# Performance work log

Hardware: AMD Instinct MI355X
Metric: run time of the kernel (lower is better)

The kernel has to match this reference:

```python
import jax, jax.numpy as jnp
import numpy as np
from math import sqrt

P = 1.0  # axis-aligned transform exponent (init arg p)
EPS = 1e-6


def setup_inputs() -> dict:
    key = jax.random.key(0)
    k1, k2, k3, k4 = jax.random.split(key, 4)
    B, L, S, H, E = 4, 2048, 2048, 8, 64
    return {
        "queries": jax.random.normal(k1, (B, L, H, E), dtype=jnp.float32),
        "keys": jax.random.normal(k2, (B, S, H, E), dtype=jnp.float32),
        "values": jax.random.normal(k3, (B, S, H, E), dtype=jnp.float32),
        "attn_mask": jnp.zeros((1, 1, 1, 1), dtype=bool),  # unused: mask_flag=False
        "directional_weights": jnp.ones((1, 1, 1, 1), dtype=jnp.float32),
        "dynamic_param": jax.random.normal(k4, (1,), dtype=jnp.float32),
    }


def _transform(x, directional_weights, dynamic_param):
    # axis_aligned_transformation: rescale by (1/std over seq dim)^p (unbiased std, like torch)
    std = jnp.std(x, axis=-2, keepdims=True, ddof=1)
    x = x * (1.0 / (std + EPS)) ** P
    # directional_reweighting then nonlinear_mapping
    x = x * directional_weights
    return jnp.tanh(x) * dynamic_param


def reference(queries, keys, values, attn_mask, directional_weights, dynamic_param):
    B, L, H, E = queries.shape
    scale = 1.0 / sqrt(E)
    qt = _transform(queries, directional_weights, dynamic_param)  # [B,L,H,E]
    kt = _transform(keys, directional_weights, dynamic_param)     # [B,S,H,E]
    scores = jnp.einsum('blhe,bshe->bhls', qt, kt)                # [B,H,L,S]
    # per-row tau = sqrt(var(scores) + eps), unbiased variance like torch.var
    tau = jnp.sqrt(jnp.var(scores, axis=-1, keepdims=True, ddof=1) + EPS)
    A = jax.nn.softmax(scale * scores / tau, axis=-1)             # [B,H,L,S]
    V = jnp.einsum('bhls,bshd->blhd', A, values)                  # [B,L,H,D]
    return V
```

## Files before the change

### kernel.cpp

```cpp
#include <hip/hip_runtime.h>
#include <math.h>

#define B_ 4
#define L_ 2048
#define S_ 2048
#define H_ 8
#define E_ 64
#define BH_ (B_*H_)
#define EPS 1e-6f

typedef __attribute__((ext_vector_type(8))) short short8;
typedef __attribute__((ext_vector_type(4))) float f32x4;

__device__ __forceinline__ unsigned short f2bf(float f) {
    unsigned int u = __float_as_uint(f);
    u = (u + 0x7fffu + ((u >> 16) & 1u)) >> 16;
    return (unsigned short)u;
}

__device__ __forceinline__ float bf2f(unsigned short u) {
    return __uint_as_float(((unsigned int)u) << 16);
}

__device__ __forceinline__ float fast_tanh(float x) {
    float e = __expf(2.0f * x);
    return 1.0f - 2.0f / (e + 1.0f);
}

__device__ __forceinline__ int swb(int row, int byteoff) {
    return row * 128 + ((((byteoff >> 4) ^ (row & 7)) << 4) | (byteoff & 15));
}

__global__ __launch_bounds__(256) void pre_kernel(
    const float* __restrict__ xq, const float* __restrict__ xk,
    const float* __restrict__ xv,
    unsigned short* __restrict__ qt, unsigned short* __restrict__ kt,
    unsigned short* __restrict__ vt,
    const float* __restrict__ dwp, const float* __restrict__ dpp)
{
    __shared__ float ls[64][65];
    int bx = blockIdx.x;
    if (bx < 4096) {
        const float* x = (bx < 2048) ? xq : xk;
        unsigned short* xt = (bx < 2048) ? qt : kt;
        int g = (bx & 2047) * 256 + threadIdx.x;
        int e = g & 63;
        int bl = g >> 6;
        int b = bl >> 11;
        int l = bl & 2047;
        size_t base = (size_t)bl * (H_ * E_) + e;
        float v[8], s = 0.f, q = 0.f;
#pragma unroll
        for (int h = 0; h < 8; ++h) {
            float t = x[base + h * E_];
            v[h] = t; s += t; q += t * t;
        }
        float mean = s * 0.125f;
        float var = (q - s * mean) * (1.f / 7.f);
        var = fmaxf(var, 0.f);
        float inv = 1.f / (sqrtf(var) + EPS);
        float wsc = dwp[0] * inv;
        float d = dpp[0];
#pragma unroll
        for (int h = 0; h < 8; ++h) {
            float t = fast_tanh(v[h] * wsc) * d;
            xt[((size_t)(b * H_ + h) * L_ + l) * E_ + e] = f2bf(t);
        }
    } else {
        int t2 = bx - 4096;
        int s0 = (t2 & 31) * 64;
        int h = (t2 >> 5) & 7, b = t2 >> 8;
        int t = threadIdx.x;
#pragma unroll
        for (int i = 0; i < 4; ++i) {
            int idx = t + i * 256;
            int r = idx >> 4, c4 = (idx & 15) * 4;
            const float4 f = *(const float4*)&xv[((size_t)(b * S_ + s0 + r) * H_ + h) * E_ + c4];
            ls[r][c4] = f.x; ls[r][c4 + 1] = f.y; ls[r][c4 + 2] = f.z; ls[r][c4 + 3] = f.w;
        }
        __syncthreads();
        size_t ob = ((size_t)(b * H_ + h) * (S_ / 64) + (s0 >> 6)) * 4096;
#pragma unroll
        for (int i = 0; i < 2; ++i) {
            int ri = t + i * 256;
            int et = ri >> 7, c = (ri >> 6) & 1, quad = (ri >> 4) & 3, m = ri & 15;
            int e = et * 16 + m, sb = c * 32 + quad * 8;
            unsigned short tmp[8];
#pragma unroll
            for (int j = 0; j < 8; ++j) tmp[j] = f2bf(ls[sb + j][e]);
            *(uint4*)&vt[ob + (size_t)ri * 8] = *(uint4*)tmp;
        }
    }
}

__global__ __launch_bounds__(256) void gram_kernel(
    const unsigned short* __restrict__ kt, unsigned short* __restrict__ Gb,
    float* __restrict__ ksum)
{
    __shared__ unsigned short ks[128 * 72];
    __shared__ float gs[4096];
    __shared__ float kss[64];
    int bh = blockIdx.x;
    const unsigned short* base = kt + (size_t)bh * S_ * E_;
    int tid = threadIdx.x, lane = tid & 63, w = tid >> 6;
    int m = lane & 15, quad = lane >> 4;

    f32x4 acc[4][4];
#pragma unroll
    for (int i = 0; i < 4; ++i)
#pragma unroll
        for (int j = 0; j < 4; ++j) acc[i][j] = (f32x4){0.f, 0.f, 0.f, 0.f};
    float ksp[4] = {0.f, 0.f, 0.f, 0.f};

    short8 stg[4];
#pragma unroll
    for (int i = 0; i < 4; ++i)
        stg[i] = *(const short8*)(base + (size_t)(tid + i * 256) * 8);

    for (int ch = 0; ch < 16; ++ch) {
        __syncthreads();
#pragma unroll
        for (int i = 0; i < 4; ++i) {
            int u = tid + i * 256;
            *(short8*)&ks[(u >> 3) * 72 + (u & 7) * 8] = stg[i];
        }
        __syncthreads();
        if (ch < 15) {
#pragma unroll
            for (int i = 0; i < 4; ++i)
                stg[i] = *(const short8*)(base + (size_t)(ch + 1) * 8192 + (tid + i * 256) * 8);
        }
        int s0 = w * 32;
        short8 af[4];
#pragma unroll
        for (int i = 0; i < 4; ++i) {
            short8 a;
#pragma unroll
            for (int kk = 0; kk < 8; ++kk) {
                unsigned short uv = ks[(s0 + quad * 8 + kk) * 72 + i * 16 + m];
                a[kk] = (short)uv;
                ksp[i] += bf2f(uv);
            }
            af[i] = a;
        }
#pragma unroll
        for (int i = 0; i < 4; ++i)
#pragma unroll
            for (int j = 0; j < 4; ++j)
                acc[i][j] = __builtin_amdgcn_mfma_f32_16x16x32_bf16(af[i], af[j], acc[i][j], 0, 0, 0);
    }
#pragma unroll
    for (int i = 0; i < 4; ++i) {
        ksp[i] += __shfl_xor(ksp[i], 16);
        ksp[i] += __shfl_xor(ksp[i], 32);
    }
    for (int w2 = 0; w2 < 4; ++w2) {
        if (w == w2) {
#pragma unroll
            for (int i = 0; i < 4; ++i)
#pragma unroll
                for (int j = 0; j < 4; ++j)
#pragma unroll
                    for (int r = 0; r < 4; ++r) {
                        int idx = (i * 16 + quad * 4 + r) * 64 + j * 16 + m;
                        if (w2 == 0) gs[idx] = acc[i][j][r]; else gs[idx] += acc[i][j][r];
                    }
            if (lane < 16) {
#pragma unroll
                for (int i = 0; i < 4; ++i) {
                    int e = i * 16 + lane;
                    if (w2 == 0) kss[e] = ksp[i]; else kss[e] += ksp[i];
                }
            }
        }
        __syncthreads();
    }
#pragma unroll
    for (int ii = 0; ii < 16; ++ii) {
        int idx = tid + ii * 256;
        Gb[(size_t)bh * 4096 + idx] = f2bf(gs[idx]);
    }
    if (tid < 64) ksum[bh * 64 + tid] = kss[tid];
}

__global__ __launch_bounds__(512, 4) void attn_kernel(
    const unsigned short* __restrict__ qt,
    const unsigned short* __restrict__ kt,
    const unsigned short* __restrict__ vt,
    const unsigned short* __restrict__ Gb,
    const float* __restrict__ ksum,
    float* __restrict__ out)
{
    __shared__ __align__(16) char lds[33792];
    const int tid = threadIdx.x;
    const int lane = tid & 63;
    const int w = tid >> 6;
    const int m = lane & 15;
    const int quad = lane >> 4;
    char* ptb = lds + 16384 + w * 2048;
    float2* ascr = (float2*)(lds + 32768) + w * 16;

    int blk = blockIdx.x;
    int bh = (blk & 7) * 4 + ((blk >> 3) & 3);
    int l0 = (blk >> 5) * 128;
    int b = bh >> 3, h = bh & 7;

    const unsigned short* qtb = qt + (size_t)bh * L_ * E_;
    const unsigned short* ktb = kt + (size_t)bh * S_ * E_;
    const unsigned short* vtb = vt + (size_t)bh * (S_ / 64) * 4096;

    short8 qf[2];
#pragma unroll
    for (int c = 0; c < 2; ++c)
        qf[c] = *(const short8*)(qtb + (size_t)(l0 + w * 16 + m) * E_ + c * 32 + quad * 8);

    float al, alm;
    {
        const unsigned short* gb = Gb + (size_t)bh * 4096;
        short8 gfr[4][2];
#pragma unroll
        for (int j = 0; j < 4; ++j)
#pragma unroll
            for (int c = 0; c < 2; ++c)
                gfr[j][c] = *(const short8*)(gb + (size_t)(j * 16 + m) * 64 + c * 32 + quad * 8);
        float ksl[4];
#pragma unroll
        for (int j = 0; j < 4; ++j) ksl[j] = ksum[bh * 64 + j * 16 + m];
        f32x4 accj[4];
#pragma unroll
        for (int j = 0; j < 4; ++j) {
            accj[j] = (f32x4){0.f, 0.f, 0.f, 0.f};
            accj[j] = __builtin_amdgcn_mfma_f32_16x16x32_bf16(qf[0], gfr[j][0], accj[j], 0, 0, 0);
            accj[j] = __builtin_amdgcn_mfma_f32_16x16x32_bf16(qf[1], gfr[j][1], accj[j], 0, 0, 0);
        }
        float ps[4] = {0, 0, 0, 0}, pr[4] = {0, 0, 0, 0};
#pragma unroll
        for (int r = 0; r < 4; ++r)
#pragma unroll
            for (int j = 0; j < 4; ++j) {
                float qv = bf2f(qtb[(size_t)(l0 + w * 16 + quad * 4 + r) * E_ + j * 16 + m]);
                ps[r] = fmaf(accj[j][r], qv, ps[r]);
                pr[r] = fmaf(qv, ksl[j], pr[r]);
            }
#pragma unroll
        for (int mask = 1; mask < 16; mask <<= 1)
#pragma unroll
            for (int r = 0; r < 4; ++r) {
                ps[r] += __shfl_xor(ps[r], mask);
                pr[r] += __shfl_xor(pr[r], mask);
            }
        if (m == 0) {
#pragma unroll
            for (int r = 0; r < 4; ++r) {
                float sum = pr[r];
                float mu = sum * (1.f / S_);
                float var = (ps[r] - sum * mu) * (1.f / (S_ - 1));
                var = fmaxf(var, 0.f);
                float tau = sqrtf(var + EPS);
                float a = 0.125f / tau;
                ascr[quad * 4 + r] = make_float2(a, a * mu);
            }
        }
        float2 a2 = ascr[m];
        al = a2.x; alm = a2.y;
    }

    float dsum = 0.f;
    f32x4 oacc[4];
#pragma unroll
    for (int et = 0; et < 4; ++et) oacc[et] = (f32x4){0.f, 0.f, 0.f, 0.f};

    int ko[4], pw[4];
#pragma unroll
    for (int nt = 0; nt < 4; ++nt) {
        ko[nt] = swb(nt * 16 + m, quad * 16);
        pw[nt] = swb(m, nt * 32 + quad * 8);
    }
    const int pr0 = swb(m, quad * 16);
    const int stg = swb(tid >> 3, (tid & 7) * 16);

    uint4 kr = *(const uint4*)(ktb + (size_t)tid * 8);
    *(uint4*)(lds + stg) = kr;
    __syncthreads();

    auto step = [&](int st, char* kcur, char* knxt) {
        if (st < S_ / 64 - 1)
            kr = *(const uint4*)(ktb + (size_t)(st + 1) * 4096 + (size_t)tid * 8);
        const unsigned short* vstb = vtb + (size_t)st * 4096;
        short8 vf[2][4];
#pragma unroll
        for (int c = 0; c < 2; ++c)
#pragma unroll
            for (int et = 0; et < 4; ++et)
                vf[c][et] = *(const short8*)(vstb + et * 1024 + c * 512 + lane * 8);

#pragma unroll
        for (int nt = 0; nt < 4; ++nt) {
            short8 kf0 = *(const short8*)(kcur + ko[nt]);
            short8 kf1 = *(const short8*)(kcur + (ko[nt] ^ 64));
            f32x4 acc = (f32x4){0.f, 0.f, 0.f, 0.f};
            acc = __builtin_amdgcn_mfma_f32_16x16x32_bf16(kf0, qf[0], acc, 0, 0, 0);
            acc = __builtin_amdgcn_mfma_f32_16x16x32_bf16(kf1, qf[1], acc, 0, 0, 0);
            unsigned int u0, u1, u2, u3;
            {
                float p0 = __expf(fmaf(al, acc[0], -alm));
                float p1 = __expf(fmaf(al, acc[1], -alm));
                float p2 = __expf(fmaf(al, acc[2], -alm));
                float p3 = __expf(fmaf(al, acc[3], -alm));
                u0 = __float_as_uint(p0) & 0xffff0000u;
                u1 = __float_as_uint(p1) & 0xffff0000u;
                u2 = __float_as_uint(p2) & 0xffff0000u;
                u3 = __float_as_uint(p3) & 0xffff0000u;
                dsum += __uint_as_float(u0) + __uint_as_float(u1)
                      + __uint_as_float(u2) + __uint_as_float(u3);
            }
            uint2 pk;
            pk.x = (u0 >> 16) | u1;
            pk.y = (u2 >> 16) | u3;
            *(uint2*)(ptb + pw[nt]) = pk;
        }
        short8 pf0 = *(const short8*)(ptb + pr0);
        short8 pf1 = *(const short8*)(ptb + (pr0 ^ 64));
#pragma unroll
        for (int et = 0; et < 4; ++et) {
            oacc[et] = __builtin_amdgcn_mfma_f32_16x16x32_bf16(pf0, vf[0][et], oacc[et], 0, 0, 0);
            oacc[et] = __builtin_amdgcn_mfma_f32_16x16x32_bf16(pf1, vf[1][et], oacc[et], 0, 0, 0);
        }
        if (st < S_ / 64 - 1)
            *(uint4*)(knxt + stg) = kr;
        __syncthreads();
    };
#pragma unroll 1
    for (int st2 = 0; st2 < S_ / 128; ++st2) {
        step(2 * st2,     lds,        lds + 8192);
        step(2 * st2 + 1, lds + 8192, lds);
    }

    dsum += __shfl_xor(dsum, 16);
    dsum += __shfl_xor(dsum, 32);
#pragma unroll
    for (int r = 0; r < 4; ++r) {
        float dn = __shfl(dsum, quad * 4 + r);
        float rd = 1.0f / dn;
        size_t row = (size_t)(b * L_ + l0 + w * 16 + quad * 4 + r);
#pragma unroll
        for (int et = 0; et < 4; ++et)
            out[(row * H_ + h) * E_ + et * 16 + m] = oacc[et][r] * rd;
    }
}

extern "C" void kernel_launch(void* const* d_in, const int* in_sizes, int n_in,
                              void* d_out, int out_size, void* d_ws, size_t ws_size,
                              hipStream_t stream)
{
    const float* q = (const float*)d_in[0];
    const float* k = (const float*)d_in[1];
    const float* v = (const float*)d_in[2];
    const float* dw = (const float*)d_in[4];
    const float* dp = (const float*)d_in[5];
    float* out = (float*)d_out;

    unsigned short* qt = (unsigned short*)d_ws;
    unsigned short* kt = qt + (size_t)BH_ * L_ * E_;
    unsigned short* vt = kt + (size_t)BH_ * S_ * E_;
    unsigned short* Gb = vt + (size_t)BH_ * E_ * S_;
    float* ksum = (float*)(Gb + (size_t)BH_ * 4096);

    pre_kernel<<<5120, 256, 0, stream>>>(q, k, v, qt, kt, vt, dw, dp);
    gram_kernel<<<BH_, 256, 0, stream>>>(kt, Gb, ksum);
    attn_kernel<<<512, 512, 0, stream>>>(qt, kt, vt, Gb, ksum, out);
}
```

Measured before the change: 171.6 us.

## Keep softmax probabilities in registers via permlane swaps and MFMA row sums

The P tile no longer makes a round trip through LDS. Probabilities are packed to bf16 with v_cvt_pk_bf16_f32 and rearranged into the MFMA A-operand layout with v_permlane32/16 swaps. Exp is now computed with native v_exp_f32 on log2e-prescaled coefficients. The row denominator is accumulated by an extra MFMA against a ones vector instead of scalar adds and shuffles. This removes LDS writes and reads per tile and shrinks shared memory, at the cost of two extra MFMAs per step and a switch from truncation to round-to-nearest bf16.

```diff
diff --git a/kernel.cpp b/kernel.cpp
--- a/kernel.cpp
+++ b/kernel.cpp
@@ -8,6 +8,7 @@
 #define E_ 64
 #define BH_ (B_*H_)
 #define EPS 1e-6f
+#define LOG2E 1.44269504088896340736f
 
 typedef __attribute__((ext_vector_type(8))) short short8;
 typedef __attribute__((ext_vector_type(4))) float f32x4;
@@ -25,6 +26,23 @@
 __device__ __forceinline__ float fast_tanh(float x) {
     float e = __expf(2.0f * x);
     return 1.0f - 2.0f / (e + 1.0f);
+}
+
+__device__ __forceinline__ unsigned int cvt_pk_bf16(float lo, float hi) {
+    unsigned int r;
+    asm("v_cvt_pk_bf16_f32 %0, %1, %2" : "=v"(r) : "v"(lo), "v"(hi));
+    return r;
+}
+__device__ __forceinline__ float exp2_fast(float x) {
+    float r;
+    asm("v_exp_f32 %0, %1" : "=v"(r) : "v"(x));
+    return r;
+}
+__device__ __forceinline__ void swap32(unsigned int &a, unsigned int &b) {
+    asm("v_permlane32_swap_b32 %0, %1" : "+v"(a), "+v"(b));
+}
+__device__ __forceinline__ void swap16(unsigned int &a, unsigned int &b) {
+    asm("v_permlane16_swap_b32 %0, %1" : "+v"(a), "+v"(b));
 }
 
 __device__ __forceinline__ int swb(int row, int byteoff) {
@@ -191,14 +209,13 @@
     const float* __restrict__ ksum,
     float* __restrict__ out)
 {
-    __shared__ __align__(16) char lds[33792];
+    __shared__ __align__(16) char lds[17408];
     const int tid = threadIdx.x;
     const int lane = tid & 63;
     const int w = tid >> 6;
     const int m = lane & 15;
     const int quad = lane >> 4;
-    char* ptb = lds + 16384 + w * 2048;
-    float2* ascr = (float2*)(lds + 32768) + w * 16;
+    float2* ascr = (float2*)(lds + 16384) + w * 16;
 
     int blk = blockIdx.x;
     int bh = (blk & 7) * 4 + ((blk >> 3) & 3);
@@ -214,7 +231,7 @@
     for (int c = 0; c < 2; ++c)
         qf[c] = *(const short8*)(qtb + (size_t)(l0 + w * 16 + m) * E_ + c * 32 + quad * 8);
 
-    float al, alm;
+    float al2, nalm2;
     {
         const unsigned short* gb = Gb + (size_t)bh * 4096;
         short8 gfr[4][2];
@@ -262,21 +279,22 @@
             }
         }
         float2 a2 = ascr[m];
-        al = a2.x; alm = a2.y;
-    }
-
-    float dsum = 0.f;
+        al2 = a2.x * LOG2E; nalm2 = -a2.y * LOG2E;
+    }
+
     f32x4 oacc[4];
 #pragma unroll
     for (int et = 0; et < 4; ++et) oacc[et] = (f32x4){0.f, 0.f, 0.f, 0.f};
-
-    int ko[4], pw[4];
-#pragma unroll
-    for (int nt = 0; nt < 4; ++nt) {
+    f32x4 asum = (f32x4){0.f, 0.f, 0.f, 0.f};
+
+    short8 ones;
+#pragma unroll
+    for (int j = 0; j < 8; ++j) ones[j] = (short)0x3F80;
+
+    int ko[4];
+#pragma unroll
+    for (int nt = 0; nt < 4; ++nt)
         ko[nt] = swb(nt * 16 + m, quad * 16);
-        pw[nt] = swb(m, nt * 32 + quad * 8);
-    }
-    const int pr0 = swb(m, quad * 16);
     const int stg = swb(tid >> 3, (tid & 7) * 16);
 
     uint4 kr = *(const uint4*)(ktb + (size_t)tid * 8);
@@ -294,6 +312,7 @@
             for (int et = 0; et < 4; ++et)
                 vf[c][et] = *(const short8*)(vstb + et * 1024 + c * 512 + lane * 8);
 
+        unsigned int W[4][2];
 #pragma unroll
         for (int nt = 0; nt < 4; ++nt) {
             short8 kf0 = *(const short8*)(kcur + ko[nt]);
@@ -301,31 +320,31 @@
             f32x4 acc = (f32x4){0.f, 0.f, 0.f, 0.f};
             acc = __builtin_amdgcn_mfma_f32_16x16x32_bf16(kf0, qf[0], acc, 0, 0, 0);
             acc = __builtin_amdgcn_mfma_f32_16x16x32_bf16(kf1, qf[1], acc, 0, 0, 0);
-            unsigned int u0, u1, u2, u3;
-            {
-                float p0 = __expf(fmaf(al, acc[0], -alm));
-                float p1 = __expf(fmaf(al, acc[1], -alm));
-                float p2 = __expf(fmaf(al, acc[2], -alm));
-                float p3 = __expf(fmaf(al, acc[3], -alm));
-                u0 = __float_as_uint(p0) & 0xffff0000u;
-                u1 = __float_as_uint(p1) & 0xffff0000u;
-                u2 = __float_as_uint(p2) & 0xffff0000u;
-                u3 = __float_as_uint(p3) & 0xffff0000u;
-                dsum += __uint_as_float(u0) + __uint_as_float(u1)
-                      + __uint_as_float(u2) + __uint_as_float(u3);
-            }
-            uint2 pk;
-            pk.x = (u0 >> 16) | u1;
-            pk.y = (u2 >> 16) | u3;
-            *(uint2*)(ptb + pw[nt]) = pk;
-        }
-        short8 pf0 = *(const short8*)(ptb + pr0);
-        short8 pf1 = *(const short8*)(ptb + (pr0 ^ 64));
+            float p0 = exp2_fast(fmaf(al2, acc[0], nalm2));
+            float p1 = exp2_fast(fmaf(al2, acc[1], nalm2));
+            float p2 = exp2_fast(fmaf(al2, acc[2], nalm2));
+            float p3 = exp2_fast(fmaf(al2, acc[3], nalm2));
+            W[nt][0] = cvt_pk_bf16(p0, p1);
+            W[nt][1] = cvt_pk_bf16(p2, p3);
+        }
+        short8 pf[2];
+#pragma unroll
+        for (int c = 0; c < 2; ++c) {
+            unsigned int a0 = W[2 * c][0], b0 = W[2 * c + 1][0];
+            unsigned int a1 = W[2 * c][1], b1 = W[2 * c + 1][1];
+            swap32(a0, b0); swap16(a0, b0);
+            swap32(a1, b1); swap16(a1, b1);
+            uint4 pk4;
+            pk4.x = a0; pk4.y = a1; pk4.z = b0; pk4.w = b1;
+            pf[c] = *(short8*)&pk4;
+        }
 #pragma unroll
         for (int et = 0; et < 4; ++et) {
-            oacc[et] = __builtin_amdgcn_mfma_f32_16x16x32_bf16(pf0, vf[0][et], oacc[et], 0, 0, 0);
-            oacc[et] = __builtin_amdgcn_mfma_f32_16x16x32_bf16(pf1, vf[1][et], oacc[et], 0, 0, 0);
-        }
+            oacc[et] = __builtin_amdgcn_mfma_f32_16x16x32_bf16(pf[0], vf[0][et], oacc[et], 0, 0, 0);
+            oacc[et] = __builtin_amdgcn_mfma_f32_16x16x32_bf16(pf[1], vf[1][et], oacc[et], 0, 0, 0);
+        }
+        asum = __builtin_amdgcn_mfma_f32_16x16x32_bf16(pf[0], ones, asum, 0, 0, 0);
+        asum = __builtin_amdgcn_mfma_f32_16x16x32_bf16(pf[1], ones, asum, 0, 0, 0);
         if (st < S_ / 64 - 1)
             *(uint4*)(knxt + stg) = kr;
         __syncthreads();
@@ -336,12 +355,9 @@
         step(2 * st2 + 1, lds + 8192, lds);
     }
 
-    dsum += __shfl_xor(dsum, 16);
-    dsum += __shfl_xor(dsum, 32);
 #pragma unroll
     for (int r = 0; r < 4; ++r) {
-        float dn = __shfl(dsum, quad * 4 + r);
-        float rd = 1.0f / dn;
+        float rd = 1.0f / asum[r];
         size_t row = (size_t)(b * L_ + l0 + w * 16 + quad * 4 + r);
 #pragma unroll
         for (int et = 0; et < 4; ++et)
```

Result: no change. 168.8 us (-1.6%).
